# Optimization experiments

Hardware: AMD Instinct MI355X
Metric: run time of the kernel (lower is better)

## Reference

```python
import jax, jax.numpy as jnp
import numpy as np
import math


def setup_inputs() -> dict:
    key = jax.random.key(0)
    k1, k2 = jax.random.split(key)
    B, C, H, W = 16, 128, 56, 56
    Cw, ks = 16, 3  # grouped dynamic weights: groups = C // Cw = 8
    x = jax.random.normal(k1, (B, C, H, W), dtype=jnp.float32)
    w = jax.random.normal(k2, (B, Cw, ks * ks, H, W), dtype=jnp.float32)
    return {"x": x, "w": w}


def reference(x, w):
    # x: [B, C, H, W]; w: [B, Cw, ks*ks, H, W] (5-D path of SKA.forward)
    B, C, H, W = x.shape
    ks_sq = w.shape[2]
    ks = int(math.isqrt(ks_sq))
    pad = (ks - 1) // 2
    Cw = w.shape[1]
    if Cw != C:
        # torch w.repeat(1, groups, 1, 1, 1) tiles along the channel dim
        w = jnp.tile(w, (1, C // Cw, 1, 1, 1))
    # Fused equivalent of unfold * w -> sum over kernel taps: accumulate
    # shifted views of the padded input weighted by per-pixel kernels.
    xp = jnp.pad(x, ((0, 0), (0, 0), (pad, pad), (pad, pad)))
    out = jnp.zeros_like(x)
    for i in range(ks):
        for j in range(ks):
            # F.unfold flattens taps row-major: k = i * ks + j
            out = out + xp[:, :, i:i + H, j:j + W] * w[:, :, i * ks + j]
    return out
```

## Files before the change

kernel.cpp:

```cpp
#include <hip/hip_runtime.h>


#define SKA_B   16
#define SKA_C   128
#define SKA_CW  16
#define SKA_H   56
#define SKA_W   56
#define SKA_HW  (SKA_H * SKA_W)
#define SKA_G   (SKA_C / SKA_CW)
#define SKA_Q   (SKA_W / 4)

__global__ __launch_bounds__(256) void ska_kernel(
    const float* __restrict__ x,
    const float* __restrict__ w,
    float* __restrict__ out)
{
    const int tid = blockIdx.x * 256 + threadIdx.x;
    const int q  = tid % SKA_Q;
    int t        = tid / SKA_Q;
    const int h  = t % SKA_H;
    t            = t / SKA_H;
    const int cw = t % SKA_CW;
    const int b  = t / SKA_CW;

    const int col = q * 4;
    const int hw  = h * SKA_W + col;

    const float* wp = w + ((size_t)(b * SKA_CW + cw) * 9) * SKA_HW + hw;
    float4 wk[9];
#pragma unroll
    for (int k = 0; k < 9; ++k) wk[k] = *(const float4*)(wp + (size_t)k * SKA_HW);

    const bool hv0 = (h > 0);
    const bool hv2 = (h < SKA_H - 1);
    const bool lv  = (q > 0);
    const bool rv  = (q < SKA_Q - 1);

    const float* xb = x   + ((size_t)b * SKA_C + cw) * SKA_HW + hw;
    float*       ob = out + ((size_t)b * SKA_C + cw) * SKA_HW + hw;

#pragma unroll
    for (int g = 0; g < SKA_G; ++g) {
        const float* xc = xb + (size_t)g * SKA_CW * SKA_HW;
        float acc0 = 0.f, acc1 = 0.f, acc2 = 0.f, acc3 = 0.f;

#pragma unroll
        for (int r = 0; r < 3; ++r) {
            if (r == 0 && !hv0) continue;
            if (r == 2 && !hv2) continue;
            const float* xr = xc + (r - 1) * SKA_W;
            const float4 m = *(const float4*)xr;
            const float  L = lv ? xr[-1] : 0.0f;
            const float  R = rv ? xr[4]  : 0.0f;
            const float4 w0 = wk[3 * r + 0];
            const float4 w1 = wk[3 * r + 1];
            const float4 w2 = wk[3 * r + 2];
            acc0 += L   * w0.x + m.x * w1.x + m.y * w2.x;
            acc1 += m.x * w0.y + m.y * w1.y + m.z * w2.y;
            acc2 += m.y * w0.z + m.z * w1.z + m.w * w2.z;
            acc3 += m.z * w0.w + m.w * w1.w + R   * w2.w;
        }

        float4 o;
        o.x = acc0; o.y = acc1; o.z = acc2; o.w = acc3;
        *(float4*)(ob + (size_t)g * SKA_CW * SKA_HW) = o;
    }
}

extern "C" void kernel_launch(void* const* d_in, const int* in_sizes, int n_in,
                              void* d_out, int out_size, void* d_ws, size_t ws_size,
                              hipStream_t stream) {
    const float* x = (const float*)d_in[0];
    const float* w = (const float*)d_in[1];
    float* out = (float*)d_out;

    const int total_threads = SKA_B * SKA_CW * SKA_H * SKA_Q;
    const int block = 256;
    const int grid = total_threads / block;

    ska_kernel<<<grid, block, 0, stream>>>(x, w, out);
}
```

Baseline: 106.9 us.

## Stage input planes in LDS with zero halo, one block per channel slice

Each block now owns one (batch, weight-channel) pair and half of the channel groups. It loads 4 full 56x56 input planes into shared memory with a zero-padded border, then computes the 3x3 dynamic conv from LDS, reloading the per-pixel weights for each block. This removes the redundant global row loads and boundary branches. In exchange the weights are read twice, occupancy is limited by roughly 63KB of LDS per block, and the grid shrinks to 512 blocks.

```diff
diff --git a/kernel.cpp b/kernel.cpp
--- a/kernel.cpp
+++ b/kernel.cpp
@@ -7,63 +7,76 @@
 #define SKA_H   56
 #define SKA_W   56
 #define SKA_HW  (SKA_H * SKA_W)
-#define SKA_G   (SKA_C / SKA_CW)
-#define SKA_Q   (SKA_W / 4)
+#define CPB     4
+#define LROWS   58
+#define LSTRIDE 68
+#define LSLOTS  (CPB * LROWS * LSTRIDE / 4)
 
 __global__ __launch_bounds__(256) void ska_kernel(
     const float* __restrict__ x,
     const float* __restrict__ w,
     float* __restrict__ out)
 {
-    const int tid = blockIdx.x * 256 + threadIdx.x;
-    const int q  = tid % SKA_Q;
-    int t        = tid / SKA_Q;
-    const int h  = t % SKA_H;
-    t            = t / SKA_H;
-    const int cw = t % SKA_CW;
-    const int b  = t / SKA_CW;
+    __shared__ float lds[CPB][LROWS][LSTRIDE];
 
-    const int col = q * 4;
-    const int hw  = h * SKA_W + col;
+    const int tid = threadIdx.x;
+    const int blk = blockIdx.x;
+    const int gs  = blk & 1;
+    const int cwb = blk >> 1;
+    const int cw  = cwb & 15;
+    const int b   = cwb >> 4;
 
-    const float* wp = w + ((size_t)(b * SKA_CW + cw) * 9) * SKA_HW + hw;
-    float4 wk[9];
+    {
+        const float4 z = {0.f, 0.f, 0.f, 0.f};
+        float4* lf4 = (float4*)&lds[0][0][0];
+        for (int i = tid; i < LSLOTS; i += 256) lf4[i] = z;
+    }
+    __syncthreads();
+
+    const float* xb = x + ((size_t)b * SKA_C + (size_t)gs * CPB * SKA_CW + cw) * SKA_HW;
+    for (int i = tid; i < CPB * SKA_H * 14; i += 256) {
+        const int q  = i % 14;
+        const int t  = i / 14;
+        const int h  = t % SKA_H;
+        const int ch = t / SKA_H;
+        const float4 v = *(const float4*)(xb + (size_t)ch * SKA_CW * SKA_HW + h * SKA_W + 4 * q);
+        *(float4*)&lds[ch][h + 1][4 * q + 4] = v;
+    }
+    __syncthreads();
+
+    const float* wb = w + ((size_t)(b * SKA_CW + cw) * 9) * SKA_HW;
+    float* ob = out + ((size_t)b * SKA_C + (size_t)gs * CPB * SKA_CW + cw) * SKA_HW;
+
+    for (int i = tid; i < SKA_H * 14; i += 256) {
+        const int q  = i % 14;
+        const int h  = i / 14;
+        const int hw = h * SKA_W + 4 * q;
+
+        float4 wk[9];
 #pragma unroll
-    for (int k = 0; k < 9; ++k) wk[k] = *(const float4*)(wp + (size_t)k * SKA_HW);
-
-    const bool hv0 = (h > 0);
-    const bool hv2 = (h < SKA_H - 1);
-    const bool lv  = (q > 0);
-    const bool rv  = (q < SKA_Q - 1);
-
-    const float* xb = x   + ((size_t)b * SKA_C + cw) * SKA_HW + hw;
-    float*       ob = out + ((size_t)b * SKA_C + cw) * SKA_HW + hw;
+        for (int k = 0; k < 9; ++k)
+            wk[k] = *(const float4*)(wb + (size_t)k * SKA_HW + hw);
 
 #pragma unroll
-    for (int g = 0; g < SKA_G; ++g) {
-        const float* xc = xb + (size_t)g * SKA_CW * SKA_HW;
-        float acc0 = 0.f, acc1 = 0.f, acc2 = 0.f, acc3 = 0.f;
-
+        for (int ch = 0; ch < CPB; ++ch) {
+            float a0 = 0.f, a1 = 0.f, a2 = 0.f, a3 = 0.f;
 #pragma unroll
-        for (int r = 0; r < 3; ++r) {
-            if (r == 0 && !hv0) continue;
-            if (r == 2 && !hv2) continue;
-            const float* xr = xc + (r - 1) * SKA_W;
-            const float4 m = *(const float4*)xr;
-            const float  L = lv ? xr[-1] : 0.0f;
-            const float  R = rv ? xr[4]  : 0.0f;
-            const float4 w0 = wk[3 * r + 0];
-            const float4 w1 = wk[3 * r + 1];
-            const float4 w2 = wk[3 * r + 2];
-            acc0 += L   * w0.x + m.x * w1.x + m.y * w2.x;
-            acc1 += m.x * w0.y + m.y * w1.y + m.z * w2.y;
-            acc2 += m.y * w0.z + m.z * w1.z + m.w * w2.z;
-            acc3 += m.z * w0.w + m.w * w1.w + R   * w2.w;
+            for (int r = 0; r < 3; ++r) {
+                const float* lp = &lds[ch][h + r][4 * q + 2];
+                const float2 dl = *(const float2*)lp;
+                const float4 m  = *(const float4*)(lp + 2);
+                const float  e  = lp[6];
+                const float4 w0 = wk[3 * r + 0];
+                const float4 w1 = wk[3 * r + 1];
+                const float4 w2 = wk[3 * r + 2];
+                a0 += dl.y * w0.x + m.x * w1.x + m.y * w2.x;
+                a1 += m.x  * w0.y + m.y * w1.y + m.z * w2.y;
+                a2 += m.y  * w0.z + m.z * w1.z + m.w * w2.z;
+                a3 += m.z  * w0.w + m.w * w1.w + e   * w2.w;
+            }
+            float4 o; o.x = a0; o.y = a1; o.z = a2; o.w = a3;
+            *(float4*)(ob + (size_t)ch * SKA_CW * SKA_HW + hw) = o;
         }
-
-        float4 o;
-        o.x = acc0; o.y = acc1; o.z = acc2; o.w = acc3;
-        *(float4*)(ob + (size_t)g * SKA_CW * SKA_HW) = o;
     }
 }
 
@@ -74,9 +87,6 @@
     const float* w = (const float*)d_in[1];
     float* out = (float*)d_out;
 
-    const int total_threads = SKA_B * SKA_CW * SKA_H * SKA_Q;
-    const int block = 256;
-    const int grid = total_threads / block;
-
-    ska_kernel<<<grid, block, 0, stream>>>(x, w, out);
+    const int grid = SKA_B * SKA_CW * 2;
+    ska_kernel<<<grid, 256, 0, stream>>>(x, w, out);
 }
```

Measured after the change: 103.3 us. 3.3% less time.

## Split group loop across threads and use nontemporal output stores

Applied to the files above, without the earlier changes.

Each thread now computes one output channel (group index folded into the thread index) instead of looping over all 8 groups, which multiplies the thread count by 8 and raises parallelism and occupancy. The cost is that each dynamic weight is reloaded once per group rather than held in registers, relying on L2 reuse. Output uses nontemporal stores to avoid cache pollution, and launch bounds request higher occupancy.

```diff
diff --git a/kernel.cpp b/kernel.cpp
--- a/kernel.cpp
+++ b/kernel.cpp
@@ -7,10 +7,11 @@
 #define SKA_H   56
 #define SKA_W   56
 #define SKA_HW  (SKA_H * SKA_W)
-#define SKA_G   (SKA_C / SKA_CW)
-#define SKA_Q   (SKA_W / 4)
+#define SKA_Q   14
 
-__global__ __launch_bounds__(256) void ska_kernel(
+typedef float f32x4 __attribute__((ext_vector_type(4)));
+
+__global__ __launch_bounds__(256, 6) void ska_kernel(
     const float* __restrict__ x,
     const float* __restrict__ w,
     float* __restrict__ out)
@@ -20,51 +21,46 @@
     int t        = tid / SKA_Q;
     const int h  = t % SKA_H;
     t            = t / SKA_H;
-    const int cw = t % SKA_CW;
-    const int b  = t / SKA_CW;
+    const int ch = t & 7;
+    t            = t >> 3;
+    const int cw = t & 15;
+    const int b  = t >> 4;
 
     const int col = q * 4;
     const int hw  = h * SKA_W + col;
 
-    const float* wp = w + ((size_t)(b * SKA_CW + cw) * 9) * SKA_HW + hw;
-    float4 wk[9];
-#pragma unroll
-    for (int k = 0; k < 9; ++k) wk[k] = *(const float4*)(wp + (size_t)k * SKA_HW);
+    const float* xc = x   + ((size_t)b * SKA_C + ch * SKA_CW + cw) * SKA_HW + hw;
+    const float* wp = w   + ((size_t)(b * SKA_CW + cw) * 9) * SKA_HW + hw;
+    float*       oc = out + ((size_t)b * SKA_C + ch * SKA_CW + cw) * SKA_HW + hw;
 
     const bool hv0 = (h > 0);
     const bool hv2 = (h < SKA_H - 1);
     const bool lv  = (q > 0);
     const bool rv  = (q < SKA_Q - 1);
 
-    const float* xb = x   + ((size_t)b * SKA_C + cw) * SKA_HW + hw;
-    float*       ob = out + ((size_t)b * SKA_C + cw) * SKA_HW + hw;
+    float a0 = 0.f, a1 = 0.f, a2 = 0.f, a3 = 0.f;
 
 #pragma unroll
-    for (int g = 0; g < SKA_G; ++g) {
-        const float* xc = xb + (size_t)g * SKA_CW * SKA_HW;
-        float acc0 = 0.f, acc1 = 0.f, acc2 = 0.f, acc3 = 0.f;
+    for (int r = 0; r < 3; ++r) {
+        if (r == 0 && !hv0) continue;
+        if (r == 2 && !hv2) continue;
+        const float* xr = xc + (r - 1) * SKA_W;
+        const float4 m = *(const float4*)xr;
+        float L = 0.f, R = 0.f;
+        if (lv) L = xr[-1];
+        if (rv) R = xr[4];
+        const float4 w0 = *(const float4*)(wp + (size_t)(3 * r + 0) * SKA_HW);
+        const float4 w1 = *(const float4*)(wp + (size_t)(3 * r + 1) * SKA_HW);
+        const float4 w2 = *(const float4*)(wp + (size_t)(3 * r + 2) * SKA_HW);
 
-#pragma unroll
-        for (int r = 0; r < 3; ++r) {
-            if (r == 0 && !hv0) continue;
-            if (r == 2 && !hv2) continue;
-            const float* xr = xc + (r - 1) * SKA_W;
-            const float4 m = *(const float4*)xr;
-            const float  L = lv ? xr[-1] : 0.0f;
-            const float  R = rv ? xr[4]  : 0.0f;
-            const float4 w0 = wk[3 * r + 0];
-            const float4 w1 = wk[3 * r + 1];
-            const float4 w2 = wk[3 * r + 2];
-            acc0 += L   * w0.x + m.x * w1.x + m.y * w2.x;
-            acc1 += m.x * w0.y + m.y * w1.y + m.z * w2.y;
-            acc2 += m.y * w0.z + m.z * w1.z + m.w * w2.z;
-            acc3 += m.z * w0.w + m.w * w1.w + R   * w2.w;
-        }
+        a0 += L   * w0.x + m.x * w1.x + m.y * w2.x;
+        a1 += m.x * w0.y + m.y * w1.y + m.z * w2.y;
+        a2 += m.y * w0.z + m.z * w1.z + m.w * w2.z;
+        a3 += m.z * w0.w + m.w * w1.w + R   * w2.w;
+    }
 
-        float4 o;
-        o.x = acc0; o.y = acc1; o.z = acc2; o.w = acc3;
-        *(float4*)(ob + (size_t)g * SKA_CW * SKA_HW) = o;
-    }
+    f32x4 o = {a0, a1, a2, a3};
+    __builtin_nontemporal_store(o, (f32x4*)oc);
 }
 
 extern "C" void kernel_launch(void* const* d_in, const int* in_sizes, int n_in,
@@ -74,7 +70,7 @@
     const float* w = (const float*)d_in[1];
     float* out = (float*)d_out;
 
-    const int total_threads = SKA_B * SKA_CW * SKA_H * SKA_Q;
+    const int total_threads = SKA_B * SKA_CW * 8 * SKA_H * SKA_Q;
     const int block = 256;
     const int grid = total_threads / block;
 
```

Result: slower. 114.3 us (+6.9%).
